# Performance work log

Measured on AMD Instinct MI355X. Metric: run time of the kernel, lower is better.

## Reference

```python
import jax, jax.numpy as jnp
import numpy as np

BN_EPS = 1e-5

def _square_distance(a, b):
    # a: (B,N,3), b: (B,M,3) -> (B,N,M) squared euclidean distance
    a2 = jnp.sum(a * a, axis=-1)[:, :, None]
    b2 = jnp.sum(b * b, axis=-1)[:, None, :]
    return a2 + b2 - 2.0 * jnp.einsum('bnd,bmd->bnm', a, b)

def _bn(x, gamma, beta, mean, var):
    # eval-mode batchnorm over channel (last) dim
    return (x - mean) * jax.lax.rsqrt(var + BN_EPS) * gamma + beta

def setup_inputs() -> dict:
    key = jax.random.key(0)
    ks = jax.random.split(key, 16)
    B, M, N, D, C = 4, 2048, 16384, 64, 64
    din, dout = C + D, 64
    return {
        'xyz_down': jax.random.normal(ks[0], (B, M, 3), jnp.float32),
        'xyz_up': jax.random.normal(ks[1], (B, N, 3), jnp.float32),
        'feat_down': jax.random.normal(ks[2], (B, M, D), jnp.float32),
        'feat_up': jax.random.normal(ks[3], (B, N, C), jnp.float32),
        'W1': jax.random.normal(ks[4], (din, din), jnp.float32) * 0.05,
        'b1': jax.random.normal(ks[5], (din,), jnp.float32) * 0.05,
        'bn1_gamma': jax.random.uniform(ks[6], (din,), jnp.float32, 0.5, 1.5),
        'bn1_beta': jax.random.normal(ks[7], (din,), jnp.float32) * 0.05,
        'bn1_mean': jax.random.normal(ks[8], (din,), jnp.float32) * 0.05,
        'bn1_var': jax.random.uniform(ks[9], (din,), jnp.float32, 0.5, 1.5),
        'W2': jax.random.normal(ks[10], (dout, din), jnp.float32) * 0.05,
        'b2': jax.random.normal(ks[11], (dout,), jnp.float32) * 0.05,
        'bn2_gamma': jax.random.uniform(ks[12], (dout,), jnp.float32, 0.5, 1.5),
        'bn2_beta': jax.random.normal(ks[13], (dout,), jnp.float32) * 0.05,
        'bn2_mean': jax.random.normal(ks[14], (dout,), jnp.float32) * 0.05,
        'bn2_var': jax.random.uniform(ks[15], (dout,), jnp.float32, 0.5, 1.5),
    }

def reference(xyz_down, xyz_up, feat_down, feat_up,
              W1, b1, bn1_gamma, bn1_beta, bn1_mean, bn1_var,
              W2, b2, bn2_gamma, bn2_beta, bn2_mean, bn2_var):
    dist = _square_distance(xyz_up, xyz_down)              # (B,N,M)
    dist_recip = 1.0 / (dist + 1e-8)
    weight = dist_recip / jnp.sum(dist_recip, axis=2, keepdims=True)
    # bmm-equivalent of the original broadcast-multiply-sum
    feat_interp = jnp.einsum('bnm,bmd->bnd', weight, feat_down)  # (B,N,D)
    x = jnp.concatenate([feat_up, feat_interp], axis=-1)   # (B,N,C+D)
    # Conv1d(k=1) == pointwise linear over channel dim
    x = jnp.einsum('bnc,oc->bno', x, W1) + b1
    x = jax.nn.relu(_bn(x, bn1_gamma, bn1_beta, bn1_mean, bn1_var))
    x = jnp.einsum('bnc,oc->bno', x, W2) + b2
    x = _bn(x, bn2_gamma, bn2_beta, bn2_mean, bn2_var)
    return x
```

## Files before the change

kernel.cpp:

```cpp
#include <hip/hip_runtime.h>

typedef unsigned short u16;
typedef unsigned int   u32;
typedef unsigned long long u64;

typedef __attribute__((ext_vector_type(8))) short bf16x8;
typedef __attribute__((ext_vector_type(4))) float f32x4;
typedef __attribute__((ext_vector_type(2))) float f32x2;

#define BB 4
#define MM 2048
#define NN 16384
#define DD 64

__device__ __forceinline__ u16 f2bf(float f) {
    union { float f; u32 u; } v; v.f = f;
    u32 r = v.u + 0x7fffu + ((v.u >> 16) & 1u);
    return (u16)(r >> 16);
}

__device__ __forceinline__ u32 pack_trunc(float hi, float lo) {
    union { float f; u32 u; } a, b; a.f = hi; b.f = lo;
    return __builtin_amdgcn_perm(a.u, b.u, 0x07060302);
}

__device__ __forceinline__ u32 pack_rne(float hi, float lo) {
    return (u32)f2bf(lo) | ((u32)f2bf(hi) << 16);
}

__device__ __forceinline__ bf16x8 pack8(float4 p, float4 q) {
    bf16x8 v;
    v[0] = (short)f2bf(p.x); v[1] = (short)f2bf(p.y);
    v[2] = (short)f2bf(p.z); v[3] = (short)f2bf(p.w);
    v[4] = (short)f2bf(q.x); v[5] = (short)f2bf(q.y);
    v[6] = (short)f2bf(q.z); v[7] = (short)f2bf(q.w);
    return v;
}

#define OFF_FDT   0ull
#define OFF_XYZP  1048576ull
#define OFF_W1S   1179648ull
#define OFF_W2S   1212416ull
#define OFF_BN    1228800ull
#define WS_NEED   1230336ull

__global__ __launch_bounds__(256)
void prep6_kernel(const float* __restrict__ xyz_down,
                  const float* __restrict__ feat_down,
                  const float* __restrict__ W1, const float* __restrict__ b1,
                  const float* __restrict__ g1, const float* __restrict__ be1,
                  const float* __restrict__ m1, const float* __restrict__ v1,
                  const float* __restrict__ W2, const float* __restrict__ b2,
                  const float* __restrict__ g2, const float* __restrict__ be2,
                  const float* __restrict__ m2, const float* __restrict__ v2,
                  u16* __restrict__ fdT, float4* __restrict__ xyzP,
                  u16* __restrict__ w1s, u16* __restrict__ w2s,
                  float* __restrict__ bnbuf)
{
    const int blk = blockIdx.x, t = threadIdx.x;
    if (blk < 256) {
        __shared__ u16 T[32 * 72];
        const int b = blk >> 6, m0 = (blk & 63) * 32;
        {
            const int row = t >> 3, seg = (t & 7) * 8;
            const float4* src = (const float4*)(feat_down + ((size_t)(b * MM + m0 + row)) * 64 + seg);
            float4 v0 = src[0], v1 = src[1];
            bf16x8 pk = pack8(v0, v1);
            *(bf16x8*)&T[row * 72 + seg] = pk;
        }
        __syncthreads();
        {
            const int d = t & 63, w = t >> 6;
            union { u16 h[8]; uint4 q; } o;
#pragma unroll
            for (int j = 0; j < 8; j++) o.h[j] = T[(w * 8 + j) * 72 + d];
            *(uint4*)&fdT[((size_t)(b * 64 + d)) * MM + m0 + w * 8] = o.q;
        }
    } else if (blk < 272) {
        int g = (blk - 256) * 256 + t;
        int b = g >> 10, p = g & 1023;
        const float* s = xyz_down + ((size_t)b * MM + 2 * p) * 3;
        float x0 = s[0], y0 = s[1], z0 = s[2];
        float x1 = s[3], y1 = s[4], z1 = s[5];
        float w0 = x0 * x0 + y0 * y0 + z0 * z0 + 1e-8f;
        float w1v = x1 * x1 + y1 * y1 + z1 * z1 + 1e-8f;
        xyzP[(size_t)g * 2 + 0] = make_float4(-2.f * x0, -2.f * x1, -2.f * y0, -2.f * y1);
        xyzP[(size_t)g * 2 + 1] = make_float4(-2.f * z0, -2.f * z1, w0, w1v);
    } else if (blk < 280) {
        int slot = (blk - 272) * 256 + t;
        int f = slot >> 6, l = slot & 63;
        int kg = f >> 3, ot = f & 7;
        int o = ot * 16 + (l & 15), c = kg * 32 + (l >> 4) * 8;
        const float4* src = (const float4*)(W1 + (size_t)o * 128 + c);
        bf16x8 v = pack8(src[0], src[1]);
        *(bf16x8*)&w1s[(size_t)slot * 8] = v;
    } else if (blk < 284) {
        int slot = (blk - 280) * 256 + t;
        int f = slot >> 6, l = slot & 63;
        int kg = f >> 2, ot = f & 3;
        int o = ot * 16 + (l & 15), c = kg * 32 + (l >> 4) * 8;
        const float4* src = (const float4*)(W2 + (size_t)o * 128 + c);
        bf16x8 v = pack8(src[0], src[1]);
        *(bf16x8*)&w2s[(size_t)slot * 8] = v;
    } else {
        if (t < 128) {
            float a = g1[t] * rsqrtf(v1[t] + 1e-5f);
            bnbuf[t] = a;
            bnbuf[128 + t] = (b1[t] - m1[t]) * a + be1[t];
        } else if (t < 192) {
            int o = t - 128;
            float a = g2[o] * rsqrtf(v2[o] + 1e-5f);
            bnbuf[256 + o] = a;
            bnbuf[320 + o] = (b2[o] - m2[o]) * a + be2[o];
        }
    }
}

__global__ __launch_bounds__(256, 2)
void fused7_kernel(const float* __restrict__ xyz_up,
                   const u16* __restrict__ fdT,
                   const float4* __restrict__ xyzP,
                   const float* __restrict__ feat_up,
                   const u16* __restrict__ w1s,
                   const u16* __restrict__ w2s,
                   const float* __restrict__ bnbuf,
                   float* __restrict__ out)
{
    __shared__ u16   ftbuf[2][64 * 72];
    __shared__ float xyzb[2][32 * 12];
    __shared__ u16   xh[128 * 136];
    __shared__ float bnl[384];

    const int tid = threadIdx.x;
    const int b  = blockIdx.x >> 7;
    const int n0 = (blockIdx.x & 127) * 128;
    const int wave = tid >> 6;
    const int lane = tid & 63;
    const int q    = lane >> 4;
    const int nl   = lane & 15;

    bnl[tid] = bnbuf[tid];
    if (tid < 128) bnl[256 + tid] = bnbuf[256 + tid];

    {
        const int r = tid >> 1, sg = (tid & 1) * 32;
        const float4* fs = (const float4*)(feat_up + ((size_t)(b * NN + n0 + r)) * 64 + sg);
        float4 f0 = fs[0], f1 = fs[1], f2 = fs[2], f3 = fs[3];
        float4 f4 = fs[4], f5 = fs[5], f6 = fs[6], f7 = fs[7];
        uint4 o0, o1;
        o0.x = pack_rne(f0.y, f0.x); o0.y = pack_rne(f0.w, f0.z);
        o0.z = pack_rne(f1.y, f1.x); o0.w = pack_rne(f1.w, f1.z);
        o1.x = pack_rne(f2.y, f2.x); o1.y = pack_rne(f2.w, f2.z);
        o1.z = pack_rne(f3.y, f3.x); o1.w = pack_rne(f3.w, f3.z);
        uint4* xd = (uint4*)&xh[r * 136 + sg];
        xd[0] = o0; xd[1] = o1;
        uint4 o2, o3;
        o2.x = pack_rne(f4.y, f4.x); o2.y = pack_rne(f4.w, f4.z);
        o2.z = pack_rne(f5.y, f5.x); o2.w = pack_rne(f5.w, f5.z);
        o3.x = pack_rne(f6.y, f6.x); o3.y = pack_rne(f6.w, f6.z);
        o3.z = pack_rne(f7.y, f7.x); o3.w = pack_rne(f7.w, f7.z);
        xd[2] = o2; xd[3] = o3;
    }

    float ax[2], ay[2], az[2];
    f32x2 a22[2];
#pragma unroll
    for (int rt = 0; rt < 2; rt++) {
        const int row = n0 + wave * 32 + rt * 16 + nl;
        const float* xu = xyz_up + ((size_t)(b * NN + row)) * 3;
        ax[rt] = xu[0]; ay[rt] = xu[1]; az[rt] = xu[2];
        float a2 = ax[rt] * ax[rt] + ay[rt] * ay[rt] + az[rt] * az[rt];
        a22[rt] = (f32x2){a2, a2};
    }
    const f32x2 eps2 = (f32x2){1e-8f, 1e-8f};

    f32x4 acc[2][4];
#pragma unroll
    for (int rt = 0; rt < 2; rt++)
#pragma unroll
        for (int i = 0; i < 4; i++) acc[rt][i] = (f32x4){0.f, 0.f, 0.f, 0.f};
    f32x4 accd[2];
    accd[0] = (f32x4){0.f, 0.f, 0.f, 0.f};
    accd[1] = (f32x4){0.f, 0.f, 0.f, 0.f};

    bf16x8 ones;
#pragma unroll
    for (int i = 0; i < 8; i++) ones[i] = (short)0x3F80;

    const int sd = tid >> 2, sms = (tid & 3) * 16;
    const u16* fsrc = fdT + ((size_t)(b * 64 + sd)) * MM + sms;
    const float4* xsrc = xyzP + ((size_t)b * 1024 + (tid >> 1)) * 2 + (tid & 1);
    float* xdst = &xyzb[0][0] + (tid >> 1) * 12 + (tid & 1) * 4;

    {
        u16* fd = &ftbuf[0][sd * 72 + sms];
        *(uint4*)fd       = *(const uint4*)(fsrc);
        *(uint4*)(fd + 8) = *(const uint4*)(fsrc + 8);
        if (tid < 64) *(float4*)xdst = xsrc[0];
    }
    __syncthreads();

    for (int c = 0; c < 32; ++c) {
        const int cur = c & 1, nxt = cur ^ 1;
        const bool have_next = (c + 1) < 32;
        uint4 nf0, nf1; float4 nx;
        if (have_next) {
            const int mc = (c + 1) * 64;
            nf0 = *(const uint4*)(fsrc + mc);
            nf1 = *(const uint4*)(fsrc + mc + 8);
            if (tid < 64) nx = xsrc[(size_t)(c + 1) * 64];
        }

#pragma unroll
        for (int kk = 0; kk < 2; kk++) {
            u32 fr[2][4];
#pragma unroll
            for (int jp = 0; jp < 4; jp++) {
                const int pi = kk * 16 + q * 4 + jp;
                const float* base = &xyzb[cur][pi * 12];
                float4 ld0 = *(const float4*)(base);
                float4 ld1 = *(const float4*)(base + 4);
                f32x2 px = (f32x2){ld0.x, ld0.y};
                f32x2 py = (f32x2){ld0.z, ld0.w};
                f32x2 pz = (f32x2){ld1.x, ld1.y};
                f32x2 pw = (f32x2){ld1.z, ld1.w};
#pragma unroll
                for (int rt = 0; rt < 2; rt++) {
                    f32x2 d = __builtin_elementwise_fma(px, (f32x2){ax[rt], ax[rt]},
                              __builtin_elementwise_fma(py, (f32x2){ay[rt], ay[rt]},
                              __builtin_elementwise_fma(pz, (f32x2){az[rt], az[rt]},
                                                        pw + a22[rt])));
                    d = __builtin_elementwise_max(d, eps2);
                    float r0 = __builtin_amdgcn_rcpf(d.x);
                    float r1 = __builtin_amdgcn_rcpf(d.y);
                    fr[rt][jp] = pack_trunc(r1, r0);
                }
            }
            bf16x8 bb[4];
#pragma unroll
            for (int dt = 0; dt < 4; dt++)
                bb[dt] = *(bf16x8*)&ftbuf[cur][(dt * 16 + nl) * 72 + kk * 32 + q * 8];
#pragma unroll
            for (int rt = 0; rt < 2; rt++) {
                union { u32 u[4]; bf16x8 v; } af;
                af.u[0] = fr[rt][0]; af.u[1] = fr[rt][1];
                af.u[2] = fr[rt][2]; af.u[3] = fr[rt][3];
#pragma unroll
                for (int dt = 0; dt < 4; dt++)
                    acc[rt][dt] = __builtin_amdgcn_mfma_f32_16x16x32_bf16(af.v, bb[dt], acc[rt][dt], 0, 0, 0);
                accd[rt] = __builtin_amdgcn_mfma_f32_16x16x32_bf16(af.v, ones, accd[rt], 0, 0, 0);
            }
        }

        if (have_next) {
            u16* fd = &ftbuf[nxt][sd * 72 + sms];
            *(uint4*)fd       = nf0;
            *(uint4*)(fd + 8) = nf1;
            if (tid < 64) *(float4*)(&xyzb[nxt][0] + (tid >> 1) * 12 + (tid & 1) * 4) = nx;
        }
        __syncthreads();
    }

#pragma unroll
    for (int rt = 0; rt < 2; rt++)
#pragma unroll
    for (int reg = 0; reg < 4; reg++) {
        float inv = 1.0f / accd[rt][reg];
        int rl = wave * 32 + rt * 16 + q * 4 + reg;
#pragma unroll
        for (int dt = 0; dt < 4; dt++)
            xh[rl * 136 + 64 + dt * 16 + nl] = f2bf(acc[rt][dt][reg] * inv);
    }

    f32x4 acc1[2][8];
#pragma unroll
    for (int rt = 0; rt < 2; rt++)
#pragma unroll
        for (int i = 0; i < 8; i++) acc1[rt][i] = (f32x4){0.f, 0.f, 0.f, 0.f};
#pragma unroll
    for (int kg = 0; kg < 4; kg++) {
        bf16x8 afr[2];
#pragma unroll
        for (int rt = 0; rt < 2; rt++)
            afr[rt] = *(bf16x8*)&xh[(wave * 32 + rt * 16 + nl) * 136 + kg * 32 + q * 8];
#pragma unroll
        for (int ot = 0; ot < 8; ot++) {
            bf16x8 bf = *(const bf16x8*)(w1s + ((size_t)(kg * 8 + ot) * 64 + lane) * 8);
            acc1[0][ot] = __builtin_amdgcn_mfma_f32_16x16x32_bf16(afr[0], bf, acc1[0][ot], 0, 0, 0);
            acc1[1][ot] = __builtin_amdgcn_mfma_f32_16x16x32_bf16(afr[1], bf, acc1[1][ot], 0, 0, 0);
        }
    }
#pragma unroll
    for (int ot = 0; ot < 8; ot++) {
        int o = ot * 16 + nl;
        float aa = bnl[o], bc = bnl[128 + o];
#pragma unroll
        for (int rt = 0; rt < 2; rt++)
#pragma unroll
        for (int reg = 0; reg < 4; reg++) {
            float v = fmaxf(fmaf(acc1[rt][ot][reg], aa, bc), 0.f);
            xh[(wave * 32 + rt * 16 + q * 4 + reg) * 136 + o] = f2bf(v);
        }
    }

    f32x4 acc2[2][4];
#pragma unroll
    for (int rt = 0; rt < 2; rt++)
#pragma unroll
        for (int i = 0; i < 4; i++) acc2[rt][i] = (f32x4){0.f, 0.f, 0.f, 0.f};
#pragma unroll
    for (int kg = 0; kg < 4; kg++) {
        bf16x8 afr[2];
#pragma unroll
        for (int rt = 0; rt < 2; rt++)
            afr[rt] = *(bf16x8*)&xh[(wave * 32 + rt * 16 + nl) * 136 + kg * 32 + q * 8];
#pragma unroll
        for (int ot = 0; ot < 4; ot++) {
            bf16x8 bf = *(const bf16x8*)(w2s + ((size_t)(kg * 4 + ot) * 64 + lane) * 8);
            acc2[0][ot] = __builtin_amdgcn_mfma_f32_16x16x32_bf16(afr[0], bf, acc2[0][ot], 0, 0, 0);
            acc2[1][ot] = __builtin_amdgcn_mfma_f32_16x16x32_bf16(afr[1], bf, acc2[1][ot], 0, 0, 0);
        }
    }
    float* of = (float*)xh;
#pragma unroll
    for (int ot = 0; ot < 4; ot++) {
        int o = ot * 16 + nl;
        float aa = bnl[256 + o], bc = bnl[320 + o];
#pragma unroll
        for (int rt = 0; rt < 2; rt++)
#pragma unroll
        for (int reg = 0; reg < 4; reg++)
            of[(wave * 32 + rt * 16 + q * 4 + reg) * 68 + o] = fmaf(acc2[rt][ot][reg], aa, bc);
    }

    {
        const int r = tid >> 1, sg = (tid & 1) * 32;
        const float4* sf = (const float4*)&of[r * 68 + sg];
        float4* dst = (float4*)(out + ((size_t)(b * NN + n0 + r)) * 64 + sg);
#pragma unroll
        for (int i = 0; i < 8; i++) dst[i] = sf[i];
    }
}

#define TN 128
#define BM 64
#define RS 72
#define FS 72

__global__ __launch_bounds__(256, 3)
void interp_kernel(const float* __restrict__ xyz_down,
                   const float* __restrict__ xyz_up,
                   const float* __restrict__ feat_down,
                   u16* __restrict__ interp_out)
{
    __shared__ u16   rbuf[TN * RS];
    __shared__ u16   ftbuf[DD * FS];
    __shared__ float xyzb[BM * 3];
    __shared__ float denp[TN * 2];
    __shared__ float invden[TN];

    const int tid = threadIdx.x;
    const int b  = blockIdx.x >> 7;
    const int n0 = (blockIdx.x & 127) * TN;

    const int nl_r = tid >> 1;
    const int half = tid & 1;
    const float* xu = xyz_up + (size_t)(b * NN + n0 + nl_r) * 3;
    const float ax = xu[0], ay = xu[1], az = xu[2];

    denp[tid] = 0.f;

    const int wave = tid >> 6;
    const int lane = tid & 63;
    const int q    = lane >> 4;
    const int nl   = lane & 15;

    f32x4 acc[2][4];
#pragma unroll
    for (int i = 0; i < 2; i++)
#pragma unroll
        for (int j = 0; j < 4; j++) acc[i][j] = (f32x4){0.f, 0.f, 0.f, 0.f};

    const int sm = (tid & 31) * 2;
    const int sd = (tid >> 5) * 8;

    for (int mc = 0; mc < MM; mc += BM) {
        __syncthreads();
        if (tid < 192) xyzb[tid] = xyz_down[(size_t)(b * MM + mc) * 3 + tid];
        {
            const float4* f0 = (const float4*)(feat_down + (size_t)(b * MM + mc + sm) * DD + sd);
            const float4* f1 = (const float4*)(feat_down + (size_t)(b * MM + mc + sm + 1) * DD + sd);
            float4 a0 = f0[0], a1 = f0[1];
            float4 b0 = f1[0], b1 = f1[1];
            float r0[8] = {a0.x, a0.y, a0.z, a0.w, a1.x, a1.y, a1.z, a1.w};
            float r1[8] = {b0.x, b0.y, b0.z, b0.w, b1.x, b1.y, b1.z, b1.w};
#pragma unroll
            for (int j = 0; j < 8; j++) {
                u32 pk = (u32)f2bf(r0[j]) | ((u32)f2bf(r1[j]) << 16);
                *(u32*)&ftbuf[(sd + j) * FS + sm] = pk;
            }
        }
        __syncthreads();
        {
            float dlc = 0.f;
#pragma unroll
            for (int s = 0; s < 4; s++) {
                bf16x8 v;
#pragma unroll
                for (int j = 0; j < 8; j++) {
                    int m = half * 32 + s * 8 + j;
                    float dx = ax - xyzb[3 * m + 0];
                    float dy = ay - xyzb[3 * m + 1];
                    float dz = az - xyzb[3 * m + 2];
                    float d = fmaf(dx, dx, fmaf(dy, dy, dz * dz)) + 1e-8f;
                    float r = __builtin_amdgcn_rcpf(d);
                    dlc += r;
                    v[j] = (short)f2bf(r);
                }
                *(bf16x8*)&rbuf[nl_r * RS + half * 32 + s * 8] = v;
            }
            denp[nl_r * 2 + half] += dlc;
        }
        __syncthreads();
        {
            const int rowbase = wave * 32;
#pragma unroll
            for (int k0 = 0; k0 < BM; k0 += 32) {
                bf16x8 a0 = *(bf16x8*)&rbuf[(rowbase + nl) * RS + k0 + q * 8];
                bf16x8 a1 = *(bf16x8*)&rbuf[(rowbase + 16 + nl) * RS + k0 + q * 8];
#pragma unroll
                for (int dt = 0; dt < 4; dt++) {
                    bf16x8 bb = *(bf16x8*)&ftbuf[(dt * 16 + nl) * FS + k0 + q * 8];
                    acc[0][dt] = __builtin_amdgcn_mfma_f32_16x16x32_bf16(a0, bb, acc[0][dt], 0, 0, 0);
                    acc[1][dt] = __builtin_amdgcn_mfma_f32_16x16x32_bf16(a1, bb, acc[1][dt], 0, 0, 0);
                }
            }
        }
    }

    __syncthreads();
    if (tid < TN) invden[tid] = 1.0f / (denp[tid * 2] + denp[tid * 2 + 1]);
    __syncthreads();
    {
        const int rowbase = wave * 32;
#pragma unroll
        for (int nt = 0; nt < 2; nt++) {
#pragma unroll
            for (int reg = 0; reg < 4; reg++) {
                int nloc = rowbase + nt * 16 + q * 4 + reg;
                float inv = invden[nloc];
                size_t gbase = (size_t)(b * NN + n0 + nloc) * DD;
#pragma unroll
                for (int dt = 0; dt < 4; dt++)
                    interp_out[gbase + dt * 16 + nl] = f2bf(acc[nt][dt][reg] * inv);
            }
        }
    }
}

#define T2 64

__global__ __launch_bounds__(256, 1)
void mlp_kernel(const float* __restrict__ feat_up,
                const u16*   __restrict__ interp,
                const float* __restrict__ W1, const float* __restrict__ b1,
                const float* __restrict__ g1, const float* __restrict__ be1,
                const float* __restrict__ m1, const float* __restrict__ v1,
                const float* __restrict__ W2, const float* __restrict__ b2,
                const float* __restrict__ g2, const float* __restrict__ be2,
                const float* __restrict__ m2, const float* __restrict__ v2,
                float* __restrict__ out)
{
    __shared__ u16 xb[T2 * 136];
    __shared__ u16 hb[T2 * 136];
    __shared__ u16 w1b[128 * 136];
    __shared__ u16 w2b[64 * 136];
    __shared__ float A1[128], Bc1[128], A2[64], Bc2[64];

    const int tid = threadIdx.x;
    const int b  = blockIdx.x >> 8;
    const int n0 = (blockIdx.x & 255) * T2;
    const int wave = tid >> 6;
    const int lane = tid & 63;
    const int q    = lane >> 4;
    const int nl   = lane & 15;

    if (tid < 128) {
        float a = g1[tid] * rsqrtf(v1[tid] + 1e-5f);
        A1[tid]  = a;
        Bc1[tid] = (b1[tid] - m1[tid]) * a + be1[tid];
    } else if (tid < 192) {
        int o = tid - 128;
        float a = g2[o] * rsqrtf(v2[o] + 1e-5f);
        A2[o]  = a;
        Bc2[o] = (b2[o] - m2[o]) * a + be2[o];
    }
    {
        const float4* src = (const float4*)(W1 + (size_t)(tid >> 1) * 128 + (tid & 1) * 64);
        u16* dst = &w1b[(tid >> 1) * 136 + (tid & 1) * 64];
#pragma unroll
        for (int i = 0; i < 8; i++)
            *(bf16x8*)(dst + 8 * i) = pack8(src[2 * i], src[2 * i + 1]);
    }
    {
        const float4* src = (const float4*)(W2 + (size_t)(tid >> 2) * 128 + (tid & 3) * 32);
        u16* dst = &w2b[(tid >> 2) * 136 + (tid & 3) * 32];
#pragma unroll
        for (int i = 0; i < 4; i++)
            *(bf16x8*)(dst + 8 * i) = pack8(src[2 * i], src[2 * i + 1]);
    }
    if (tid < 128) {
        int n = tid >> 1, hf = tid & 1;
        const float4* src = (const float4*)(feat_up + (size_t)(b * NN + n0 + n) * 64 + hf * 32);
        u16* dst = &xb[n * 136 + hf * 32];
#pragma unroll
        for (int i = 0; i < 4; i++)
            *(bf16x8*)(dst + 8 * i) = pack8(src[2 * i], src[2 * i + 1]);
    } else {
        int t2 = tid - 128;
        int n = t2 >> 1, hf = t2 & 1;
        const uint4* src = (const uint4*)(interp + (size_t)(b * NN + n0 + n) * 64 + hf * 32);
        u16* dst = &xb[n * 136 + 64 + hf * 32];
#pragma unroll
        for (int i = 0; i < 4; i++)
            *(uint4*)(dst + 8 * i) = src[i];
    }
    __syncthreads();

    f32x4 acc1[8];
#pragma unroll
    for (int i = 0; i < 8; i++) acc1[i] = (f32x4){0.f, 0.f, 0.f, 0.f};
#pragma unroll
    for (int k0 = 0; k0 < 128; k0 += 32) {
        bf16x8 a = *(bf16x8*)&xb[(wave * 16 + nl) * 136 + k0 + q * 8];
#pragma unroll
        for (int ot = 0; ot < 8; ot++) {
            bf16x8 bb = *(bf16x8*)&w1b[(ot * 16 + nl) * 136 + k0 + q * 8];
            acc1[ot] = __builtin_amdgcn_mfma_f32_16x16x32_bf16(a, bb, acc1[ot], 0, 0, 0);
        }
    }
#pragma unroll
    for (int ot = 0; ot < 8; ot++) {
        int o = ot * 16 + nl;
        float aa = A1[o], bc = Bc1[o];
#pragma unroll
        for (int reg = 0; reg < 4; reg++) {
            float v = fmaxf(fmaf(acc1[ot][reg], aa, bc), 0.f);
            hb[(wave * 16 + q * 4 + reg) * 136 + o] = f2bf(v);
        }
    }
    __syncthreads();

    f32x4 acc2[4];
#pragma unroll
    for (int i = 0; i < 4; i++) acc2[i] = (f32x4){0.f, 0.f, 0.f, 0.f};
#pragma unroll
    for (int k0 = 0; k0 < 128; k0 += 32) {
        bf16x8 a = *(bf16x8*)&hb[(wave * 16 + nl) * 136 + k0 + q * 8];
#pragma unroll
        for (int ot = 0; ot < 4; ot++) {
            bf16x8 bb = *(bf16x8*)&w2b[(ot * 16 + nl) * 136 + k0 + q * 8];
            acc2[ot] = __builtin_amdgcn_mfma_f32_16x16x32_bf16(a, bb, acc2[ot], 0, 0, 0);
        }
    }
#pragma unroll
    for (int ot = 0; ot < 4; ot++) {
        int o = ot * 16 + nl;
        float aa = A2[o], bc = Bc2[o];
#pragma unroll
        for (int reg = 0; reg < 4; reg++)
            out[(size_t)(b * NN + n0 + wave * 16 + q * 4 + reg) * 64 + o] =
                fmaf(acc2[ot][reg], aa, bc);
    }
}

extern "C" void kernel_launch(void* const* d_in, const int* in_sizes, int n_in,
                              void* d_out, int out_size, void* d_ws, size_t ws_size,
                              hipStream_t stream) {
    const float* xyz_down  = (const float*)d_in[0];
    const float* xyz_up    = (const float*)d_in[1];
    const float* feat_down = (const float*)d_in[2];
    const float* feat_up   = (const float*)d_in[3];
    const float* W1  = (const float*)d_in[4];
    const float* b1  = (const float*)d_in[5];
    const float* g1  = (const float*)d_in[6];
    const float* be1 = (const float*)d_in[7];
    const float* m1  = (const float*)d_in[8];
    const float* v1  = (const float*)d_in[9];
    const float* W2  = (const float*)d_in[10];
    const float* b2  = (const float*)d_in[11];
    const float* g2  = (const float*)d_in[12];
    const float* be2 = (const float*)d_in[13];
    const float* m2  = (const float*)d_in[14];
    const float* v2  = (const float*)d_in[15];
    float* out = (float*)d_out;
    char* ws = (char*)d_ws;

    if (ws_size >= WS_NEED) {
        u16*    fdT   = (u16*)(ws + OFF_FDT);
        float4* xyzP  = (float4*)(ws + OFF_XYZP);
        u16*    w1s   = (u16*)(ws + OFF_W1S);
        u16*    w2s   = (u16*)(ws + OFF_W2S);
        float*  bnbuf = (float*)(ws + OFF_BN);

        prep6_kernel<<<dim3(285), dim3(256), 0, stream>>>(
            xyz_down, feat_down, W1, b1, g1, be1, m1, v1,
            W2, b2, g2, be2, m2, v2, fdT, xyzP, w1s, w2s, bnbuf);
        fused7_kernel<<<dim3(BB * (NN / 128)), dim3(256), 0, stream>>>(
            xyz_up, fdT, xyzP, feat_up, w1s, w2s, bnbuf, out);
    } else {
        u16* interp = (u16*)d_ws;
        interp_kernel<<<dim3(BB * (NN / TN)), dim3(256), 0, stream>>>(
            xyz_down, xyz_up, feat_down, interp);
        mlp_kernel<<<dim3(BB * (NN / T2)), dim3(256), 0, stream>>>(
            feat_up, interp, W1, b1, g1, be1, m1, v1,
            W2, b2, g2, be2, m2, v2, out);
    }
}
```

Baseline: 149.9 us.

## Alias interp and MLP shared memory to raise occupancy, shrink prep grid

The fused kernel's shared memory is now one dynamic buffer in which the MLP input tile overlays the double-buffered feature/xyz staging used during interpolation. This cuts LDS per block so launch bounds can request 4 blocks per CU instead of 2. The feat_up load moves after the interpolation loop, because the aliased region is only free once that loop ends. The prep kernel also runs fewer blocks, each converting four 32-row tiles. The tighter register budget may cause spills, and the late feat_up load is no longer overlapped with interpolation compute.

```diff
diff --git a/kernel.cpp b/kernel.cpp
--- a/kernel.cpp
+++ b/kernel.cpp
@@ -45,7 +45,7 @@
 #define WS_NEED   1230336ull
 
 __global__ __launch_bounds__(256)
-void prep6_kernel(const float* __restrict__ xyz_down,
+void prep7_kernel(const float* __restrict__ xyz_down,
                   const float* __restrict__ feat_down,
                   const float* __restrict__ W1, const float* __restrict__ b1,
                   const float* __restrict__ g1, const float* __restrict__ be1,
@@ -58,26 +58,30 @@
                   float* __restrict__ bnbuf)
 {
     const int blk = blockIdx.x, t = threadIdx.x;
-    if (blk < 256) {
+    if (blk < 64) {
         __shared__ u16 T[32 * 72];
-        const int b = blk >> 6, m0 = (blk & 63) * 32;
-        {
-            const int row = t >> 3, seg = (t & 7) * 8;
-            const float4* src = (const float4*)(feat_down + ((size_t)(b * MM + m0 + row)) * 64 + seg);
-            float4 v0 = src[0], v1 = src[1];
-            bf16x8 pk = pack8(v0, v1);
-            *(bf16x8*)&T[row * 72 + seg] = pk;
-        }
-        __syncthreads();
-        {
-            const int d = t & 63, w = t >> 6;
-            union { u16 h[8]; uint4 q; } o;
-#pragma unroll
-            for (int j = 0; j < 8; j++) o.h[j] = T[(w * 8 + j) * 72 + d];
-            *(uint4*)&fdT[((size_t)(b * 64 + d)) * MM + m0 + w * 8] = o.q;
-        }
-    } else if (blk < 272) {
-        int g = (blk - 256) * 256 + t;
+        const int b = blk >> 4, base = (blk & 15) * 128;
+#pragma unroll
+        for (int s = 0; s < 4; s++) {
+            const int m0 = base + s * 32;
+            {
+                const int row = t >> 3, seg = (t & 7) * 8;
+                const float4* src = (const float4*)(feat_down + ((size_t)(b * MM + m0 + row)) * 64 + seg);
+                float4 v0 = src[0], v1 = src[1];
+                *(bf16x8*)&T[row * 72 + seg] = pack8(v0, v1);
+            }
+            __syncthreads();
+            {
+                const int d = t & 63, w = t >> 6;
+                union { u16 h[8]; uint4 q; } o;
+#pragma unroll
+                for (int j = 0; j < 8; j++) o.h[j] = T[(w * 8 + j) * 72 + d];
+                *(uint4*)&fdT[((size_t)(b * 64 + d)) * MM + m0 + w * 8] = o.q;
+            }
+            __syncthreads();
+        }
+    } else if (blk < 80) {
+        int g = (blk - 64) * 256 + t;
         int b = g >> 10, p = g & 1023;
         const float* s = xyz_down + ((size_t)b * MM + 2 * p) * 3;
         float x0 = s[0], y0 = s[1], z0 = s[2];
@@ -86,22 +90,20 @@
         float w1v = x1 * x1 + y1 * y1 + z1 * z1 + 1e-8f;
         xyzP[(size_t)g * 2 + 0] = make_float4(-2.f * x0, -2.f * x1, -2.f * y0, -2.f * y1);
         xyzP[(size_t)g * 2 + 1] = make_float4(-2.f * z0, -2.f * z1, w0, w1v);
-    } else if (blk < 280) {
-        int slot = (blk - 272) * 256 + t;
+    } else if (blk < 88) {
+        int slot = (blk - 80) * 256 + t;
         int f = slot >> 6, l = slot & 63;
         int kg = f >> 3, ot = f & 7;
         int o = ot * 16 + (l & 15), c = kg * 32 + (l >> 4) * 8;
         const float4* src = (const float4*)(W1 + (size_t)o * 128 + c);
-        bf16x8 v = pack8(src[0], src[1]);
-        *(bf16x8*)&w1s[(size_t)slot * 8] = v;
-    } else if (blk < 284) {
-        int slot = (blk - 280) * 256 + t;
+        *(bf16x8*)&w1s[(size_t)slot * 8] = pack8(src[0], src[1]);
+    } else if (blk < 92) {
+        int slot = (blk - 88) * 256 + t;
         int f = slot >> 6, l = slot & 63;
         int kg = f >> 2, ot = f & 3;
         int o = ot * 16 + (l & 15), c = kg * 32 + (l >> 4) * 8;
         const float4* src = (const float4*)(W2 + (size_t)o * 128 + c);
-        bf16x8 v = pack8(src[0], src[1]);
-        *(bf16x8*)&w2s[(size_t)slot * 8] = v;
+        *(bf16x8*)&w2s[(size_t)slot * 8] = pack8(src[0], src[1]);
     } else {
         if (t < 128) {
             float a = g1[t] * rsqrtf(v1[t] + 1e-5f);
@@ -116,8 +118,12 @@
     }
 }
 
-__global__ __launch_bounds__(256, 2)
-void fused7_kernel(const float* __restrict__ xyz_up,
+#define SMEM_BYTES 36352
+#define FT_STRIDE  4608
+#define XY_STRIDE  1536
+
+__global__ __launch_bounds__(256, 4)
+void fused8_kernel(const float* __restrict__ xyz_up,
                    const u16* __restrict__ fdT,
                    const float4* __restrict__ xyzP,
                    const float* __restrict__ feat_up,
@@ -126,10 +132,11 @@
                    const float* __restrict__ bnbuf,
                    float* __restrict__ out)
 {
-    __shared__ u16   ftbuf[2][64 * 72];
-    __shared__ float xyzb[2][32 * 12];
-    __shared__ u16   xh[128 * 136];
-    __shared__ float bnl[384];
+    extern __shared__ char smem[];
+    float* bnl    = (float*)smem;
+    u16*   ftbase = (u16*)(smem + 1536);
+    char*  xybase = smem + 19968;
+    u16*   xh     = (u16*)(smem + 1536);
 
     const int tid = threadIdx.x;
     const int b  = blockIdx.x >> 7;
@@ -142,26 +149,6 @@
     bnl[tid] = bnbuf[tid];
     if (tid < 128) bnl[256 + tid] = bnbuf[256 + tid];
 
-    {
-        const int r = tid >> 1, sg = (tid & 1) * 32;
-        const float4* fs = (const float4*)(feat_up + ((size_t)(b * NN + n0 + r)) * 64 + sg);
-        float4 f0 = fs[0], f1 = fs[1], f2 = fs[2], f3 = fs[3];
-        float4 f4 = fs[4], f5 = fs[5], f6 = fs[6], f7 = fs[7];
-        uint4 o0, o1;
-        o0.x = pack_rne(f0.y, f0.x); o0.y = pack_rne(f0.w, f0.z);
-        o0.z = pack_rne(f1.y, f1.x); o0.w = pack_rne(f1.w, f1.z);
-        o1.x = pack_rne(f2.y, f2.x); o1.y = pack_rne(f2.w, f2.z);
-        o1.z = pack_rne(f3.y, f3.x); o1.w = pack_rne(f3.w, f3.z);
-        uint4* xd = (uint4*)&xh[r * 136 + sg];
-        xd[0] = o0; xd[1] = o1;
-        uint4 o2, o3;
-        o2.x = pack_rne(f4.y, f4.x); o2.y = pack_rne(f4.w, f4.z);
-        o2.z = pack_rne(f5.y, f5.x); o2.w = pack_rne(f5.w, f5.z);
-        o3.x = pack_rne(f6.y, f6.x); o3.y = pack_rne(f6.w, f6.z);
-        o3.z = pack_rne(f7.y, f7.x); o3.w = pack_rne(f7.w, f7.z);
-        xd[2] = o2; xd[3] = o3;
-    }
-
     float ax[2], ay[2], az[2];
     f32x2 a22[2];
 #pragma unroll
@@ -190,19 +177,21 @@
     const int sd = tid >> 2, sms = (tid & 3) * 16;
     const u16* fsrc = fdT + ((size_t)(b * 64 + sd)) * MM + sms;
     const float4* xsrc = xyzP + ((size_t)b * 1024 + (tid >> 1)) * 2 + (tid & 1);
-    float* xdst = &xyzb[0][0] + (tid >> 1) * 12 + (tid & 1) * 4;
+    const int xoff = ((tid >> 1) * 12 + (tid & 1) * 4) * 4;
 
     {
-        u16* fd = &ftbuf[0][sd * 72 + sms];
+        u16* fd = ftbase + sd * 72 + sms;
         *(uint4*)fd       = *(const uint4*)(fsrc);
         *(uint4*)(fd + 8) = *(const uint4*)(fsrc + 8);
-        if (tid < 64) *(float4*)xdst = xsrc[0];
+        if (tid < 64) *(float4*)(xybase + xoff) = xsrc[0];
     }
     __syncthreads();
 
     for (int c = 0; c < 32; ++c) {
         const int cur = c & 1, nxt = cur ^ 1;
         const bool have_next = (c + 1) < 32;
+        u16*   ftc = ftbase + cur * FT_STRIDE;
+        float* xyc = (float*)(xybase + cur * XY_STRIDE);
         uint4 nf0, nf1; float4 nx;
         if (have_next) {
             const int mc = (c + 1) * 64;
@@ -217,7 +206,7 @@
 #pragma unroll
             for (int jp = 0; jp < 4; jp++) {
                 const int pi = kk * 16 + q * 4 + jp;
-                const float* base = &xyzb[cur][pi * 12];
+                const float* base = xyc + pi * 12;
                 float4 ld0 = *(const float4*)(base);
                 float4 ld1 = *(const float4*)(base + 4);
                 f32x2 px = (f32x2){ld0.x, ld0.y};
@@ -239,7 +228,7 @@
             bf16x8 bb[4];
 #pragma unroll
             for (int dt = 0; dt < 4; dt++)
-                bb[dt] = *(bf16x8*)&ftbuf[cur][(dt * 16 + nl) * 72 + kk * 32 + q * 8];
+                bb[dt] = *(bf16x8*)(ftc + (dt * 16 + nl) * 72 + kk * 32 + q * 8);
 #pragma unroll
             for (int rt = 0; rt < 2; rt++) {
                 union { u32 u[4]; bf16x8 v; } af;
@@ -253,12 +242,30 @@
         }
 
         if (have_next) {
-            u16* fd = &ftbuf[nxt][sd * 72 + sms];
+            u16* fd = ftbase + nxt * FT_STRIDE + sd * 72 + sms;
             *(uint4*)fd       = nf0;
             *(uint4*)(fd + 8) = nf1;
-            if (tid < 64) *(float4*)(&xyzb[nxt][0] + (tid >> 1) * 12 + (tid & 1) * 4) = nx;
+            if (tid < 64) *(float4*)(xybase + nxt * XY_STRIDE + xoff) = nx;
         }
         __syncthreads();
+    }
+
+    {
+        const int r = tid >> 1, sg = (tid & 1) * 32;
+        const float4* fs = (const float4*)(feat_up + ((size_t)(b * NN + n0 + r)) * 64 + sg);
+        float4 f0 = fs[0], f1 = fs[1], f2 = fs[2], f3 = fs[3];
+        float4 f4 = fs[4], f5 = fs[5], f6 = fs[6], f7 = fs[7];
+        uint4 o0, o1, o2, o3;
+        o0.x = pack_rne(f0.y, f0.x); o0.y = pack_rne(f0.w, f0.z);
+        o0.z = pack_rne(f1.y, f1.x); o0.w = pack_rne(f1.w, f1.z);
+        o1.x = pack_rne(f2.y, f2.x); o1.y = pack_rne(f2.w, f2.z);
+        o1.z = pack_rne(f3.y, f3.x); o1.w = pack_rne(f3.w, f3.z);
+        o2.x = pack_rne(f4.y, f4.x); o2.y = pack_rne(f4.w, f4.z);
+        o2.z = pack_rne(f5.y, f5.x); o2.w = pack_rne(f5.w, f5.z);
+        o3.x = pack_rne(f6.y, f6.x); o3.y = pack_rne(f6.w, f6.z);
+        o3.z = pack_rne(f7.y, f7.x); o3.w = pack_rne(f7.w, f7.z);
+        uint4* xd = (uint4*)&xh[r * 136 + sg];
+        xd[0] = o0; xd[1] = o1; xd[2] = o2; xd[3] = o3;
     }
 
 #pragma unroll
@@ -603,10 +610,10 @@
         u16*    w2s   = (u16*)(ws + OFF_W2S);
         float*  bnbuf = (float*)(ws + OFF_BN);
 
-        prep6_kernel<<<dim3(285), dim3(256), 0, stream>>>(
+        prep7_kernel<<<dim3(93), dim3(256), 0, stream>>>(
             xyz_down, feat_down, W1, b1, g1, be1, m1, v1,
             W2, b2, g2, be2, m2, v2, fdT, xyzP, w1s, w2s, bnbuf);
-        fused7_kernel<<<dim3(BB * (NN / 128)), dim3(256), 0, stream>>>(
+        fused8_kernel<<<dim3(BB * (NN / 128)), dim3(256), SMEM_BYTES, stream>>>(
             xyz_up, fdT, xyzP, feat_up, w1s, w2s, bnbuf, out);
     } else {
         u16* interp = (u16*)d_ws;
```

Result: slower. 155.5 us (+3.7%).
